# Kernel tuning notes

Hardware: AMD Instinct MI355X
Metric: run time of the kernel (lower is better)

Reference implementation:

```python
import jax, jax.numpy as jnp
import numpy as np

B, C, TX, TY = 32, 384, 512, 2048
NL, K = 2, 3
EPS = 1e-5


def _ln(x, g, b):
    # channel-wise LayerNorm over dim 1 of [B, C, T]
    m = jnp.mean(x, axis=1, keepdims=True)
    v = jnp.mean((x - m) ** 2, axis=1, keepdims=True)
    return (x - m) * jax.lax.rsqrt(v + EPS) * g[None, :, None] + b[None, :, None]


def _conv(x, w, b):
    # x: [B, C, T], w: [O, I, K] -> 'SAME' padding == kernel_size // 2 for odd K
    y = jax.lax.conv_general_dilated(x, w, (1,), 'SAME',
                                     dimension_numbers=('NCH', 'OIH', 'NCH'))
    return y + b[None, :, None]


def _variance_predictor(x, mask, lng, lnb, cw, cb, ow, ob):
    # NL x (LayerNorm -> Conv1d -> SiLU -> [dropout=identity in eval]) * mask
    for i in range(NL):
        h = _conv(_ln(x, lng[i], lnb[i]), cw[i], cb[i])
        x = jax.nn.silu(h) * mask
    return _conv(x, ow, ob) * mask  # [B, 1, T]


def setup_inputs() -> dict:
    key = jax.random.key(0)
    it = iter(jax.random.split(key, 16))
    s = 0.02
    d = {}
    d['x'] = jax.random.normal(next(it), (B, C, TX), jnp.float32)
    d['x_mask'] = jnp.ones((B, 1, TX), jnp.float32)
    d['y_mask'] = jnp.ones((B, 1, TY), jnp.float32)
    d['pitch'] = jax.random.normal(next(it), (B, C, TY), jnp.float32)
    d['energy'] = jax.random.normal(next(it), (B, C, TY), jnp.float32)
    d['path'] = jax.random.uniform(next(it), (B, TX, TY), jnp.float32)
    for p in ('dur', 'pit', 'ene'):
        d[p + '_lng'] = jnp.ones((NL, C), jnp.float32)
        d[p + '_lnb'] = jnp.zeros((NL, C), jnp.float32)
        d[p + '_cw'] = jax.random.normal(next(it), (NL, C, C, K), jnp.float32) * s
        d[p + '_cb'] = jnp.zeros((NL, C), jnp.float32)
        d[p + '_ow'] = jax.random.normal(next(it), (1, C, 1), jnp.float32) * s
        d[p + '_ob'] = jnp.zeros((1,), jnp.float32)
    return d


def reference(x, x_mask, y_mask, pitch, energy, path,
              dur_lng, dur_lnb, dur_cw, dur_cb, dur_ow, dur_ob,
              pit_lng, pit_lnb, pit_cw, pit_cb, pit_ow, pit_ob,
              ene_lng, ene_lnb, ene_cw, ene_cb, ene_ow, ene_ob):
    dur_pred = _variance_predictor(x, x_mask, dur_lng, dur_lnb, dur_cw, dur_cb, dur_ow, dur_ob)
    # LengthRegulator: bmm against duration path matrix [B, TX, TY]
    xe = jnp.einsum('bct,bty->bcy', x, path)  # [B, C, TY]
    pitch_pred = _variance_predictor(xe, y_mask, pit_lng, pit_lnb, pit_cw, pit_cb, pit_ow, pit_ob)
    energy_pred = _variance_predictor(xe, y_mask, ene_lng, ene_lnb, ene_cw, ene_cb, ene_ow, ene_ob)
    out = xe + pitch + energy
    return (out, dur_pred, pitch_pred, energy_pred)
```

## Files before the change

### kernel.cpp

```cpp
#include <hip/hip_runtime.h>

#define B_ 32
#define C_ 384
#define TX_ 512
#define TY_ 2048
#define EPS_ 1e-5f
#define LAY_ ((size_t)(36 * 1536 * 8))

typedef __attribute__((ext_vector_type(8))) short short8;
typedef __attribute__((ext_vector_type(4))) float f32x4;

#define MFMA(a, b, c) __builtin_amdgcn_mfma_f32_16x16x32_bf16(a, b, c, 0, 0, 0)

#define WAITV(N) do { asm volatile("s_waitcnt vmcnt(" #N ")"); \
                      __builtin_amdgcn_sched_barrier(0); } while (0)
#define WAITL()  do { asm volatile("s_waitcnt lgkmcnt(0)"); \
                      __builtin_amdgcn_sched_barrier(0); } while (0)

typedef unsigned int u32;
__device__ __forceinline__ void gl_lds16(const void* g, void* l) {
    __builtin_amdgcn_global_load_lds(
        (const __attribute__((address_space(1))) u32*)g,
        (__attribute__((address_space(3))) u32*)l, 16, 0, 0);
}

__device__ inline unsigned short f2bf(float f) {
    union { float f; unsigned int u; } v; v.f = f;
    unsigned int r = v.u + 0x7fffu + ((v.u >> 16) & 1u);
    return (unsigned short)(r >> 16);
}
__device__ inline float bf2f(unsigned short s) {
    union { float f; unsigned int u; } v; v.u = ((unsigned int)s) << 16;
    return v.f;
}

template<bool INBF>
__device__ inline float ldx(const void* p, size_t i) {
    if constexpr (INBF) return bf2f(((const unsigned short*)p)[i]);
    else return ((const float*)p)[i];
}

__global__ __launch_bounds__(256) void pack_w2(const float* cw0, const float* cw1,
                                               const float* cw2, const float* g0,
                                               const float* g1, const float* g2,
                                               unsigned short* wp) {
    int idx = blockIdx.x * 256 + threadIdx.x;
    const int NG = 6 * 36 * 384 * 4;
    if (idx >= NG) return;
    int lg = idx & 3;
    int o = (idx >> 2) % 384;
    int c = ((idx >> 2) / 384) % 36;
    int lay = (idx >> 2) / (384 * 36);
    int k = c / 12, ib = c % 12;
    int pr = lay >> 1, l = lay & 1;
    const float* cw = ((pr == 0) ? cw0 : (pr == 1) ? cw1 : cw2) + (size_t)l * C_ * C_ * 3;
    const float* g  = ((pr == 0) ? g0  : (pr == 1) ? g1  : g2)  + (size_t)l * C_;
    const int i0 = ib * 32 + lg * 8;
    short8 v;
    #pragma unroll
    for (int e = 0; e < 8; e++)
        v[e] = (short)f2bf(cw[((size_t)o * C_ + i0 + e) * 3 + k] * g[i0 + e]);
    *(short8*)&wp[(size_t)idx * 8] = v;
}

__global__ __launch_bounds__(256) void bias_fold(
    const float* cw0, const float* cw1, const float* cw2,
    const float* be0, const float* be1, const float* be2,
    const float* cb0, const float* cb1, const float* cb2,
    float* biasT, float* bc0, float* bc2) {
    int idx = blockIdx.x * 256 + threadIdx.x;
    if (idx >= 6 * 384) return;
    int o = idx % 384, lay = idx / 384;
    int pr = lay >> 1, l = lay & 1;
    const float* cw = ((pr == 0) ? cw0 : (pr == 1) ? cw1 : cw2)
                      + (size_t)l * C_ * C_ * 3 + (size_t)o * C_ * 3;
    const float* be = ((pr == 0) ? be0 : (pr == 1) ? be1 : be2) + (size_t)l * C_;
    const float* cb = ((pr == 0) ? cb0 : (pr == 1) ? cb1 : cb2) + (size_t)l * C_;
    float s0 = 0.f, s1 = 0.f, s2 = 0.f;
    for (int i = 0; i < C_; i++) {
        const float b = be[i];
        s0 += cw[i * 3 + 0] * b; s1 += cw[i * 3 + 1] * b; s2 += cw[i * 3 + 2] * b;
    }
    biasT[idx] = cb[o] + s0 + s1 + s2;
    bc0[idx] = s0; bc2[idx] = s2;
}

__global__ __launch_bounds__(256) void pack_x2(const float* x, unsigned short* xp) {
    int idx = blockIdx.x * 256 + threadIdx.x;
    const int NG = B_ * 16 * 384 * 4;
    if (idx >= NG) return;
    int lg = idx & 3;
    int c = (idx >> 2) % 384;
    int q = ((idx >> 2) / 384) % 16;
    int b = (idx >> 2) / (384 * 16);
    const float* src = x + ((size_t)b * C_ + c) * TX_ + q * 32 + lg * 8;
    short8 v;
    #pragma unroll
    for (int e = 0; e < 8; e++) v[e] = (short)f2bf(src[e]);
    *(short8*)&xp[(size_t)idx * 8] = v;
}

__global__ __launch_bounds__(256) void ln_stats_f32(const float* x, float2* st, int T) {
    __shared__ float r1[4][64], r2[4][64];
    int b = blockIdx.y, t0 = blockIdx.x * 64;
    int tl = threadIdx.x & 63, g = threadIdx.x >> 6;
    int t = t0 + tl;
    const float* p = x + (size_t)b * C_ * T + t;
    float s = 0.f, ss = 0.f;
    for (int c = g; c < C_; c += 4) { float v = p[(size_t)c * T]; s += v; ss += v * v; }
    r1[g][tl] = s; r2[g][tl] = ss;
    __syncthreads();
    if (threadIdx.x < 64) {
        float s1 = r1[0][tl] + r1[1][tl] + r1[2][tl] + r1[3][tl];
        float s2 = r2[0][tl] + r2[1][tl] + r2[2][tl] + r2[3][tl];
        float m = s1 * (1.f / C_);
        float var = s2 * (1.f / C_) - m * m;
        st[(size_t)b * T + t0 + tl] = make_float2(m, rsqrtf(var + EPS_));
    }
}

template<bool INBF>
__global__ __launch_bounds__(512, 2) void fused_vp(
    const void* __restrict__ Xin, const float2* __restrict__ stin,
    const unsigned short* __restrict__ W2lay,
    const float* __restrict__ bT,
    const float* __restrict__ c0v, const float* __restrict__ c2v,
    const float* __restrict__ mask,
    float* __restrict__ pred, const float* __restrict__ ow,
    const float* __restrict__ obias, int T)
{
    __shared__ __align__(16) unsigned short xs[132 * 384];
    __shared__ __align__(16) unsigned short wlds[8][2][1536];
    __shared__ float red[260];
    __shared__ float2 st2[130];

    const int tid = threadIdx.x;
    const int b = blockIdx.y;
    const int t0 = blockIdx.x * 128;
    const int lane = tid & 63;
    const int wave = tid >> 6;
    const int lr = lane & 15, lg = lane >> 4;
    const int wm = wave * 48;

    const unsigned short* gbw = W2lay + (size_t)((wm + lr) * 4 + lg) * 8;
    const unsigned short* gbw2 = gbw + LAY_;
    auto STAGE = [&](const unsigned short* base, int c, int buf) {
        #pragma unroll
        for (int fm = 0; fm < 3; fm++)
            gl_lds16(base + (size_t)c * 12288 + fm * 512, &wlds[wave][buf][fm * 512]);
    };
    STAGE(gbw, 0, 0);
    STAGE(gbw, 1, 1);

    {
        const int tl = tid & 127;
        const int tt = 2 + tl;
        const int t = t0 + tl;
        const float2 mr = stin[(size_t)b * T + t];
        const int cg0 = (tid >> 7) * 12;
        for (int i = 0; i < 12; i++) {
            const int cg = cg0 + i;
            const size_t base = ((size_t)b * C_ + cg * 8) * T + t;
            short8 v8;
            #pragma unroll
            for (int j = 0; j < 8; j++)
                v8[j] = (short)f2bf((ldx<INBF>(Xin, base + (size_t)j * T) - mr.x) * mr.y);
            const int ph = (cg & ~7) | ((cg ^ tt) & 7);
            *(short8*)&xs[tt * 384 + ph * 8] = v8;
        }
        if (tid < 192) {
            const int q = tid / 48;
            const int tt2 = (q < 2) ? q : 128 + q;
            const int cg = tid % 48;
            const int t2 = t0 - 2 + tt2;
            short8 v8;
            if (t2 >= 0 && t2 < T) {
                const float2 mr2 = stin[(size_t)b * T + t2];
                const size_t base = ((size_t)b * C_ + cg * 8) * T + t2;
                #pragma unroll
                for (int j = 0; j < 8; j++)
                    v8[j] = (short)f2bf((ldx<INBF>(Xin, base + (size_t)j * T) - mr2.x) * mr2.y);
            } else {
                #pragma unroll
                for (int j = 0; j < 8; j++) v8[j] = 0;
            }
            const int ph = (cg & ~7) | ((cg ^ tt2) & 7);
            *(short8*)&xs[tt2 * 384 + ph * 8] = v8;
        }
    }
    __syncthreads();

    f32x4 acc[3][9];
    const f32x4 zero = {0.f, 0.f, 0.f, 0.f};
    #pragma unroll
    for (int fm = 0; fm < 3; fm++)
        #pragma unroll
        for (int fn = 0; fn < 9; fn++) acc[fm][fn] = zero;

    for (int c = 0; c < 36; ++c) {
        WAITV(3);
        short8 af[3], bf[9];
        #pragma unroll
        for (int fm = 0; fm < 3; fm++)
            af[fm] = *(const short8*)&wlds[wave][c & 1][fm * 512 + lane * 8];
        const int k = c / 12, ib = c - k * 12;
        const int cgi = ib * 4 + lg;
        #pragma unroll
        for (int fn = 0; fn < 8; fn++) {
            const int row = 1 + fn * 16 + lr + k;
            const int ph = (cgi & ~7) | ((cgi ^ row) & 7);
            bf[fn] = *(const short8*)&xs[row * 384 + ph * 8];
        }
        {
            const int row = (lr == 1) ? (129 + k) : k;
            const int ph = (cgi & ~7) | ((cgi ^ row) & 7);
            bf[8] = *(const short8*)&xs[row * 384 + ph * 8];
        }
        WAITL();
        if (c < 34) STAGE(gbw, c + 2, c & 1);
        else        STAGE(gbw2, c - 34, c & 1);
        __builtin_amdgcn_sched_barrier(0);
        __builtin_amdgcn_s_setprio(1);
        #pragma unroll
        for (int fm = 0; fm < 3; fm++)
            #pragma unroll
            for (int fn = 0; fn < 9; fn++)
                acc[fm][fn] = MFMA(af[fm], bf[fn], acc[fm][fn]);
        __builtin_amdgcn_s_setprio(0);
    }

    __syncthreads();
    if (tid < 260) red[tid] = 0.f;
    __syncthreads();

    #pragma unroll
    for (int fn = 0; fn < 8; fn++) {
        const int tt_h = 1 + fn * 16 + lr;
        const int t = t0 + fn * 16 + lr;
        const float mk = mask[(size_t)b * T + t];
        float s1 = 0.f, s2 = 0.f;
        #pragma unroll
        for (int fm = 0; fm < 3; fm++) {
            const int o0 = wm + fm * 16 + lg * 4;
            #pragma unroll
            for (int j = 0; j < 4; j++) {
                float h = acc[fm][fn][j] + bT[o0 + j];
                if (t == 0) h -= c0v[o0 + j];
                if (t == T - 1) h -= c2v[o0 + j];
                const float y = h * (1.f / (1.f + __expf(-h))) * mk;
                acc[fm][fn][j] = y;
                s1 += y; s2 += y * y;
            }
        }
        atomicAdd(&red[tt_h * 2], s1);
        atomicAdd(&red[tt_h * 2 + 1], s2);
    }
    {
        const int tt_h = (lr == 1) ? 129 : 0;
        const int t = t0 - 1 + tt_h;
        const bool inr = (lr < 2) && (t >= 0) && (t < T);
        const float mk = inr ? mask[(size_t)b * T + t] : 0.f;
        float s1 = 0.f, s2 = 0.f;
        #pragma unroll
        for (int fm = 0; fm < 3; fm++) {
            const int o0 = wm + fm * 16 + lg * 4;
            #pragma unroll
            for (int j = 0; j < 4; j++) {
                const float h = acc[fm][8][j] + bT[o0 + j];
                const float y = inr ? (h * (1.f / (1.f + __expf(-h))) * mk) : 0.f;
                acc[fm][8][j] = y;
                s1 += y; s2 += y * y;
            }
        }
        if (inr) {
            atomicAdd(&red[tt_h * 2], s1);
            atomicAdd(&red[tt_h * 2 + 1], s2);
        }
    }
    __syncthreads();

    if (tid < 130) {
        const float s1 = red[tid * 2], s2 = red[tid * 2 + 1];
        const float m = s1 * (1.f / C_);
        const float var = s2 * (1.f / C_) - m * m;
        st2[tid] = make_float2(m, rsqrtf(var + EPS_));
    }
    __syncthreads();

    #pragma unroll
    for (int fn = 0; fn < 8; fn++) {
        const int tt_h = 1 + fn * 16 + lr;
        const float2 mr = st2[tt_h];
        #pragma unroll
        for (int fm = 0; fm < 3; fm++) {
            ushort4 pk;
            #pragma unroll
            for (int j = 0; j < 4; j++)
                ((unsigned short*)&pk)[j] = f2bf((acc[fm][fn][j] - mr.x) * mr.y);
            const int cg = ((wm + fm * 16) >> 3) + (lg >> 1);
            const int ph = (cg & ~7) | ((cg ^ tt_h) & 7);
            *(ushort4*)&xs[tt_h * 384 + ph * 8 + (lg & 1) * 4] = pk;
        }
    }
    if (lr < 2) {
        const int tt_h = (lr == 1) ? 129 : 0;
        const float2 mr = st2[tt_h];
        #pragma unroll
        for (int fm = 0; fm < 3; fm++) {
            ushort4 pk;
            #pragma unroll
            for (int j = 0; j < 4; j++)
                ((unsigned short*)&pk)[j] = f2bf((acc[fm][8][j] - mr.x) * mr.y);
            const int cg = ((wm + fm * 16) >> 3) + (lg >> 1);
            const int ph = (cg & ~7) | ((cg ^ tt_h) & 7);
            *(ushort4*)&xs[tt_h * 384 + ph * 8 + (lg & 1) * 4] = pk;
        }
    }
    __syncthreads();

    f32x4 acc2[3][8];
    #pragma unroll
    for (int fm = 0; fm < 3; fm++)
        #pragma unroll
        for (int fn = 0; fn < 8; fn++) acc2[fm][fn] = zero;

    for (int c = 0; c < 36; ++c) {
        WAITV(3);
        short8 af[3], bf[8];
        #pragma unroll
        for (int fm = 0; fm < 3; fm++)
            af[fm] = *(const short8*)&wlds[wave][c & 1][fm * 512 + lane * 8];
        const int k = c / 12, ib = c - k * 12;
        const int cgi = ib * 4 + lg;
        #pragma unroll
        for (int fn = 0; fn < 8; fn++) {
            const int row = fn * 16 + lr + k;
            const int ph = (cgi & ~7) | ((cgi ^ row) & 7);
            bf[fn] = *(const short8*)&xs[row * 384 + ph * 8];
        }
        WAITL();
        STAGE(gbw2, (c + 2 < 36) ? c + 2 : 35, c & 1);
        __builtin_amdgcn_sched_barrier(0);
        __builtin_amdgcn_s_setprio(1);
        #pragma unroll
        for (int fm = 0; fm < 3; fm++)
            #pragma unroll
            for (int fn = 0; fn < 8; fn++)
                acc2[fm][fn] = MFMA(af[fm], bf[fn], acc2[fm][fn]);
        __builtin_amdgcn_s_setprio(0);
    }

    __syncthreads();
    if (tid < 128) red[tid] = 0.f;
    __syncthreads();
    #pragma unroll
    for (int fn = 0; fn < 8; fn++) {
        const int tl = fn * 16 + lr;
        const int t = t0 + tl;
        const float mk = mask[(size_t)b * T + t];
        float s1 = 0.f;
        #pragma unroll
        for (int fm = 0; fm < 3; fm++) {
            const int o0 = wm + fm * 16 + lg * 4;
            #pragma unroll
            for (int j = 0; j < 4; j++) {
                float h = acc2[fm][fn][j] + bT[384 + o0 + j];
                if (t == 0) h -= c0v[384 + o0 + j];
                if (t == T - 1) h -= c2v[384 + o0 + j];
                const float y = h * (1.f / (1.f + __expf(-h))) * mk;
                s1 += y * ow[o0 + j];
            }
        }
        atomicAdd(&red[tl], s1);
    }
    __syncthreads();
    if (tid < 128) {
        const int t = t0 + tid;
        pred[(size_t)b * T + t] = (red[tid] + obias[0]) * mask[(size_t)b * T + t];
    }
}

__global__ __launch_bounds__(512, 4) void bmm_ln(
    const unsigned short* __restrict__ x2, const float* __restrict__ path,
    const float* __restrict__ pitch, const float* __restrict__ energy,
    float* __restrict__ out, unsigned short* __restrict__ xebf,
    float2* __restrict__ stout, int fused)
{
    __shared__ __align__(16) unsigned short ps[32 * 512];
    __shared__ __align__(16) unsigned short wlds[8][2][1536];
    const int tid = threadIdx.x;
    const int bid = blockIdx.x;
    const int work = (bid & 7) * 256 + (bid >> 3);
    const int b = work >> 6;
    const int y0 = (work & 63) << 5;
    const int lane = tid & 63;
    const int wave = tid >> 6;
    const int lr = lane & 15, lg = lane >> 4;
    const int wm = wave * 48;

    const unsigned short* gbx = x2 + ((size_t)b * 16 * 1536 + (size_t)((wm + lr) * 4 + lg)) * 8;
    auto STAGE = [&](int u, int buf) {
        #pragma unroll
        for (int fm = 0; fm < 3; fm++)
            gl_lds16(gbx + (size_t)u * 12288 + fm * 512, &wlds[wave][buf][fm * 512]);
    };
    STAGE(0, 0);
    STAGE(1, 1);

    {
        const int yy = lane & 31;
        const int half = lane >> 5;
        const int gbase = (wave * 2 + half) * 4;
        const float* pb = path + (size_t)b * TX_ * TY_ + y0 + yy;
        float vv[4][8];
        #pragma unroll
        for (int i = 0; i < 4; i++) {
            const int cg = gbase + i;
            #pragma unroll
            for (int j = 0; j < 8; j++) vv[i][j] = pb[(size_t)(cg * 8 + j) * TY_];
        }
        #pragma unroll
        for (int i = 0; i < 4; i++) {
            const int cg = gbase + i;
            short8 v8;
            #pragma unroll
            for (int j = 0; j < 8; j++) v8[j] = (short)f2bf(vv[i][j]);
            const int ph = (cg & ~7) | ((cg ^ yy) & 7);
            *(short8*)&ps[yy * 512 + ph * 8] = v8;
        }
    }
    __syncthreads();

    f32x4 acc[3][2];
    const f32x4 zero = {0.f, 0.f, 0.f, 0.f};
    #pragma unroll
    for (int fm = 0; fm < 3; fm++) { acc[fm][0] = zero; acc[fm][1] = zero; }

    for (int u = 0; u < 16; ++u) {
        WAITV(3);
        short8 af[3], bf[2];
        #pragma unroll
        for (int fm = 0; fm < 3; fm++)
            af[fm] = *(const short8*)&wlds[wave][u & 1][fm * 512 + lane * 8];
        const int cgi = u * 4 + lg;
        #pragma unroll
        for (int fn = 0; fn < 2; fn++) {
            const int row = fn * 16 + lr;
            const int ph = (cgi & ~7) | ((cgi ^ row) & 7);
            bf[fn] = *(const short8*)&ps[row * 512 + ph * 8];
        }
        WAITL();
        STAGE((u + 2 < 16) ? u + 2 : 15, u & 1);
        __builtin_amdgcn_sched_barrier(0);
        __builtin_amdgcn_s_setprio(1);
        #pragma unroll
        for (int fm = 0; fm < 3; fm++) {
            acc[fm][0] = MFMA(af[fm], bf[0], acc[fm][0]);
            acc[fm][1] = MFMA(af[fm], bf[1], acc[fm][1]);
        }
        __builtin_amdgcn_s_setprio(0);
    }
    WAITV(0);

    __syncthreads();
    float* red = (float*)ps;
    if (tid < 64) red[tid] = 0.f;
    __syncthreads();

    #pragma unroll
    for (int fn = 0; fn < 2; fn++) {
        const int yl = fn * 16 + lr;
        const int y = y0 + yl;
        float s1 = 0.f, s2 = 0.f;
        #pragma unroll
        for (int fm = 0; fm < 3; fm++) {
            #pragma unroll
            for (int j = 0; j < 4; j++) {
                const int c = wm + fm * 16 + lg * 4 + j;
                const size_t gi = ((size_t)b * C_ + c) * TY_ + y;
                const float v = acc[fm][fn][j];
                if (fused) {
                    out[gi] = v + pitch[gi] + energy[gi];
                    xebf[gi] = f2bf(v);
                } else {
                    out[gi] = v;
                }
                s1 += v; s2 += v * v;
            }
        }
        atomicAdd(&red[yl * 2], s1);
        atomicAdd(&red[yl * 2 + 1], s2);
    }
    __syncthreads();
    if (tid < 32) {
        const int y = y0 + tid;
        const float s1 = red[tid * 2], s2 = red[tid * 2 + 1];
        const float m = s1 * (1.f / C_);
        const float var = s2 * (1.f / C_) - m * m;
        stout[(size_t)b * TY_ + y] = make_float2(m, rsqrtf(var + EPS_));
    }
}

__global__ __launch_bounds__(256) void add3(float4* o, const float4* p, const float4* e, int n4) {
    for (int i = blockIdx.x * 256 + threadIdx.x; i < n4; i += gridDim.x * 256) {
        float4 a = o[i], x1 = p[i], x2 = e[i];
        a.x += x1.x + x2.x; a.y += x1.y + x2.y;
        a.z += x1.z + x2.z; a.w += x1.w + x2.w;
        o[i] = a;
    }
}

extern "C" void kernel_launch(void* const* d_in, const int* in_sizes, int n_in,
                              void* d_out, int out_size, void* d_ws, size_t ws_size,
                              hipStream_t stream)
{
    const float* x      = (const float*)d_in[0];
    const float* x_mask = (const float*)d_in[1];
    const float* y_mask = (const float*)d_in[2];
    const float* pitch  = (const float*)d_in[3];
    const float* energy = (const float*)d_in[4];
    const float* path   = (const float*)d_in[5];
    const float* prm[3][6];
    for (int p = 0; p < 3; p++)
        for (int q = 0; q < 6; q++)
            prm[p][q] = (const float*)d_in[6 + p * 6 + q];

    float* out         = (float*)d_out;
    float* dur_pred    = out + (size_t)B_ * C_ * TY_;
    float* pitch_pred  = dur_pred + B_ * TX_;
    float* energy_pred = pitch_pred + B_ * TY_;

    const size_t BCTY = (size_t)B_ * C_ * TY_;
    char* w = (char*)d_ws;
    auto alloc = [&](size_t bytes) { char* r = w; w += (bytes + 255) & ~(size_t)255; return r; };

    unsigned short* W2   = (unsigned short*)alloc(6 * LAY_ * 2);
    float* biasT         = (float*)alloc(6 * 384 * 4);
    float* bc0           = (float*)alloc(6 * 384 * 4);
    float* bc2           = (float*)alloc(6 * 384 * 4);
    float2* stA          = (float2*)alloc((size_t)B_ * TY_ * 8);
    unsigned short* x2p  = (unsigned short*)alloc((size_t)B_ * 196608 * 2);
    size_t base_end = (size_t)(w - (char*)d_ws);
    unsigned short* xebf = (unsigned short*)alloc(BCTY * 2);
    size_t xe_end = (size_t)(w - (char*)d_ws);

    const bool haveXe = (xe_end <= ws_size);
    if (base_end > ws_size) return;

    pack_w2<<<dim3((6 * 36 * 384 * 4 + 255) / 256), 256, 0, stream>>>(
        prm[0][2], prm[1][2], prm[2][2], prm[0][0], prm[1][0], prm[2][0], W2);
    bias_fold<<<dim3(9), 256, 0, stream>>>(
        prm[0][2], prm[1][2], prm[2][2], prm[0][1], prm[1][1], prm[2][1],
        prm[0][3], prm[1][3], prm[2][3], biasT, bc0, bc2);
    pack_x2<<<dim3((B_ * 16 * 384 * 4 + 255) / 256), 256, 0, stream>>>(x, x2p);
    ln_stats_f32<<<dim3(TX_ / 64, B_), 256, 0, stream>>>(x, stA, TX_);

    fused_vp<false><<<dim3(TX_ / 128, B_), 512, 0, stream>>>(
        x, stA, W2, biasT, bc0, bc2, x_mask,
        dur_pred, prm[0][4], prm[0][5], TX_);

    bmm_ln<<<dim3(2048, 1, 1), 512, 0, stream>>>(
        x2p, path, pitch, energy, out, haveXe ? xebf : nullptr, stA, haveXe ? 1 : 0);

    if (haveXe) {
        fused_vp<true><<<dim3(TY_ / 128, B_), 512, 0, stream>>>(
            xebf, stA, W2 + 2 * LAY_, biasT + 2 * 384, bc0 + 2 * 384, bc2 + 2 * 384,
            y_mask, pitch_pred, prm[1][4], prm[1][5], TY_);
        fused_vp<true><<<dim3(TY_ / 128, B_), 512, 0, stream>>>(
            xebf, stA, W2 + 4 * LAY_, biasT + 4 * 384, bc0 + 4 * 384, bc2 + 4 * 384,
            y_mask, energy_pred, prm[2][4], prm[2][5], TY_);
    } else {
        fused_vp<false><<<dim3(TY_ / 128, B_), 512, 0, stream>>>(
            out, stA, W2 + 2 * LAY_, biasT + 2 * 384, bc0 + 2 * 384, bc2 + 2 * 384,
            y_mask, pitch_pred, prm[1][4], prm[1][5], TY_);
        fused_vp<false><<<dim3(TY_ / 128, B_), 512, 0, stream>>>(
            out, stA, W2 + 4 * LAY_, biasT + 4 * 384, bc0 + 4 * 384, bc2 + 4 * 384,
            y_mask, energy_pred, prm[2][4], prm[2][5], TY_);
        add3<<<dim3(2048), 256, 0, stream>>>((float4*)out, (const float4*)pitch,
                                             (const float4*)energy, B_ * C_ * TY_ / 4);
    }
}
```

Measured before the change: 643.9 us.

## Widen bmm_ln tile to 128 columns and vectorize epilogue via LDS transpose

The length-regulator bmm now computes 128 output columns per block instead of 32, so each staged weight tile of x is reused across four times as many MFMA columns and the grid drops to 512 blocks. The path matrix is staged in two 256-row halves to fit LDS. The epilogue is restructured to transpose accumulators through LDS in four rounds, so out, pitch, energy and the bf16 copy are written and read as coalesced float4/ushort4 instead of strided scalars. In exchange it uses more registers (24 accumulator tiles), lowers occupancy to 2 blocks per CU, and adds extra barriers.

After: 593.3 us. 7.9% less time.

```diff
diff --git a/kernel.cpp b/kernel.cpp
--- a/kernel.cpp
+++ b/kernel.cpp
@@ -380,119 +380,150 @@
     }
 }
 
-__global__ __launch_bounds__(512, 4) void bmm_ln(
+__global__ __launch_bounds__(512, 2) void bmm_ln(
     const unsigned short* __restrict__ x2, const float* __restrict__ path,
     const float* __restrict__ pitch, const float* __restrict__ energy,
     float* __restrict__ out, unsigned short* __restrict__ xebf,
     float2* __restrict__ stout, int fused)
 {
-    __shared__ __align__(16) unsigned short ps[32 * 512];
+    __shared__ __align__(16) unsigned short ps[128 * 256];
     __shared__ __align__(16) unsigned short wlds[8][2][1536];
+    __shared__ float red[256];
     const int tid = threadIdx.x;
     const int bid = blockIdx.x;
-    const int work = (bid & 7) * 256 + (bid >> 3);
-    const int b = work >> 6;
-    const int y0 = (work & 63) << 5;
+    const int work = (bid & 7) * 64 + (bid >> 3);
+    const int b = work >> 4;
+    const int y0 = (work & 15) << 7;
     const int lane = tid & 63;
     const int wave = tid >> 6;
     const int lr = lane & 15, lg = lane >> 4;
     const int wm = wave * 48;
 
     const unsigned short* gbx = x2 + ((size_t)b * 16 * 1536 + (size_t)((wm + lr) * 4 + lg)) * 8;
-    auto STAGE = [&](int u, int buf) {
+    auto STAGEW = [&](int u, int buf) {
         #pragma unroll
         for (int fm = 0; fm < 3; fm++)
             gl_lds16(gbx + (size_t)u * 12288 + fm * 512, &wlds[wave][buf][fm * 512]);
     };
-    STAGE(0, 0);
-    STAGE(1, 1);
-
-    {
-        const int yy = lane & 31;
-        const int half = lane >> 5;
-        const int gbase = (wave * 2 + half) * 4;
-        const float* pb = path + (size_t)b * TX_ * TY_ + y0 + yy;
-        float vv[4][8];
-        #pragma unroll
-        for (int i = 0; i < 4; i++) {
-            const int cg = gbase + i;
-            #pragma unroll
-            for (int j = 0; j < 8; j++) vv[i][j] = pb[(size_t)(cg * 8 + j) * TY_];
-        }
-        #pragma unroll
-        for (int i = 0; i < 4; i++) {
-            const int cg = gbase + i;
+    STAGEW(0, 0);
+    STAGEW(1, 1);
+
+    auto STAGEP = [&](int s) {
+        const int yy = tid & 127;
+        const int tg = tid >> 7;
+        const float* pb = path + ((size_t)b * TX_ + s * 256 + tg * 64) * TY_ + y0 + yy;
+        #pragma unroll
+        for (int g = 0; g < 8; g++) {
+            float vv[8];
+            #pragma unroll
+            for (int j = 0; j < 8; j++) vv[j] = pb[(size_t)(g * 8 + j) * TY_];
             short8 v8;
             #pragma unroll
-            for (int j = 0; j < 8; j++) v8[j] = (short)f2bf(vv[i][j]);
+            for (int j = 0; j < 8; j++) v8[j] = (short)f2bf(vv[j]);
+            const int cg = tg * 8 + g;
             const int ph = (cg & ~7) | ((cg ^ yy) & 7);
-            *(short8*)&ps[yy * 512 + ph * 8] = v8;
-        }
-    }
-    __syncthreads();
-
-    f32x4 acc[3][2];
+            *(short8*)&ps[yy * 256 + ph * 8] = v8;
+        }
+    };
+
+    f32x4 acc[3][8];
     const f32x4 zero = {0.f, 0.f, 0.f, 0.f};
     #pragma unroll
-    for (int fm = 0; fm < 3; fm++) { acc[fm][0] = zero; acc[fm][1] = zero; }
-
-    for (int u = 0; u < 16; ++u) {
-        WAITV(3);
-        short8 af[3], bf[2];
+    for (int fm = 0; fm < 3; fm++)
+        #pragma unroll
+        for (int fn = 0; fn < 8; fn++) acc[fm][fn] = zero;
+
+    for (int s = 0; s < 2; ++s) {
+        if (s) __syncthreads();
+        STAGEP(s);
+        __syncthreads();
+        for (int uu = 0; uu < 8; ++uu) {
+            const int u = s * 8 + uu;
+            WAITV(3);
+            short8 af[3], bf[8];
+            #pragma unroll
+            for (int fm = 0; fm < 3; fm++)
+                af[fm] = *(const short8*)&wlds[wave][u & 1][fm * 512 + lane * 8];
+            const int cgi = uu * 4 + lg;
+            #pragma unroll
+            for (int fn = 0; fn < 8; fn++) {
+                const int row = fn * 16 + lr;
+                const int ph = (cgi & ~7) | ((cgi ^ row) & 7);
+                bf[fn] = *(const short8*)&ps[row * 256 + ph * 8];
+            }
+            WAITL();
+            STAGEW((u + 2 < 16) ? u + 2 : 15, u & 1);
+            __builtin_amdgcn_sched_barrier(0);
+            __builtin_amdgcn_s_setprio(1);
+            #pragma unroll
+            for (int fm = 0; fm < 3; fm++)
+                #pragma unroll
+                for (int fn = 0; fn < 8; fn++)
+                    acc[fm][fn] = MFMA(af[fm], bf[fn], acc[fm][fn]);
+            __builtin_amdgcn_s_setprio(0);
+        }
+    }
+    WAITV(0);
+
+    __syncthreads();
+    if (tid < 256) red[tid] = 0.f;
+    __syncthreads();
+    #pragma unroll
+    for (int fn = 0; fn < 8; fn++) {
+        const int yl = fn * 16 + lr;
+        float s1 = 0.f, s2 = 0.f;
         #pragma unroll
         for (int fm = 0; fm < 3; fm++)
-            af[fm] = *(const short8*)&wlds[wave][u & 1][fm * 512 + lane * 8];
-        const int cgi = u * 4 + lg;
-        #pragma unroll
-        for (int fn = 0; fn < 2; fn++) {
-            const int row = fn * 16 + lr;
-            const int ph = (cgi & ~7) | ((cgi ^ row) & 7);
-            bf[fn] = *(const short8*)&ps[row * 512 + ph * 8];
-        }
-        WAITL();
-        STAGE((u + 2 < 16) ? u + 2 : 15, u & 1);
-        __builtin_amdgcn_sched_barrier(0);
-        __builtin_amdgcn_s_setprio(1);
-        #pragma unroll
-        for (int fm = 0; fm < 3; fm++) {
-            acc[fm][0] = MFMA(af[fm], bf[0], acc[fm][0]);
-            acc[fm][1] = MFMA(af[fm], bf[1], acc[fm][1]);
-        }
-        __builtin_amdgcn_s_setprio(0);
-    }
-    WAITV(0);
-
-    __syncthreads();
-    float* red = (float*)ps;
-    if (tid < 64) red[tid] = 0.f;
-    __syncthreads();
-
-    #pragma unroll
-    for (int fn = 0; fn < 2; fn++) {
-        const int yl = fn * 16 + lr;
-        const int y = y0 + yl;
-        float s1 = 0.f, s2 = 0.f;
-        #pragma unroll
-        for (int fm = 0; fm < 3; fm++) {
             #pragma unroll
             for (int j = 0; j < 4; j++) {
-                const int c = wm + fm * 16 + lg * 4 + j;
-                const size_t gi = ((size_t)b * C_ + c) * TY_ + y;
                 const float v = acc[fm][fn][j];
-                if (fused) {
-                    out[gi] = v + pitch[gi] + energy[gi];
-                    xebf[gi] = f2bf(v);
-                } else {
-                    out[gi] = v;
-                }
                 s1 += v; s2 += v * v;
             }
-        }
         atomicAdd(&red[yl * 2], s1);
         atomicAdd(&red[yl * 2 + 1], s2);
     }
-    __syncthreads();
-    if (tid < 32) {
+
+    float* psf = (float*)ps;
+    for (int r = 0; r < 4; ++r) {
+        __syncthreads();
+        if ((wave >> 1) == r) {
+            const int cbase = (wave & 1) * 48;
+            #pragma unroll
+            for (int fn = 0; fn < 8; fn++) {
+                const int yl = fn * 16 + lr;
+                #pragma unroll
+                for (int fm = 0; fm < 3; fm++) {
+                    const int cl = cbase + fm * 16 + lg * 4;
+                    #pragma unroll
+                    for (int j = 0; j < 4; j++)
+                        psf[(cl + j) * 128 + yl] = acc[fm][fn][j];
+                }
+            }
+        }
+        __syncthreads();
+        for (int idx = tid; idx < 96 * 32; idx += 512) {
+            const int cl = idx >> 5;
+            const int y4 = idx & 31;
+            const int c = 96 * r + cl;
+            const size_t gi = ((size_t)b * C_ + c) * TY_ + y0 + y4 * 4;
+            float4 v = ((float4*)&psf[cl * 128])[y4];
+            if (fused) {
+                const float4 p = *(const float4*)&pitch[gi];
+                const float4 e = *(const float4*)&energy[gi];
+                float4 o;
+                o.x = v.x + p.x + e.x; o.y = v.y + p.y + e.y;
+                o.z = v.z + p.z + e.z; o.w = v.w + p.w + e.w;
+                *(float4*)&out[gi] = o;
+                ushort4 xb;
+                xb.x = f2bf(v.x); xb.y = f2bf(v.y); xb.z = f2bf(v.z); xb.w = f2bf(v.w);
+                *(ushort4*)&xebf[gi] = xb;
+            } else {
+                *(float4*)&out[gi] = v;
+            }
+        }
+    }
+    __syncthreads();
+    if (tid < 128) {
         const int y = y0 + tid;
         const float s1 = red[tid * 2], s2 = red[tid * 2 + 1];
         const float m = s1 * (1.f / C_);
@@ -559,7 +590,7 @@
         x, stA, W2, biasT, bc0, bc2, x_mask,
         dur_pred, prm[0][4], prm[0][5], TX_);
 
-    bmm_ln<<<dim3(2048, 1, 1), 512, 0, stream>>>(
+    bmm_ln<<<dim3(512, 1, 1), 512, 0, stream>>>(
         x2p, path, pitch, energy, out, haveXe ? xebf : nullptr, stA, haveXe ? 1 : 0);
 
     if (haveXe) {
```
